# Kernel tuning notes

Measured on AMD Instinct MI355X. Metric: run time of the kernel, lower is better.

Reference implementation:

```python
import jax, jax.numpy as jnp
import numpy as np

B, C, H, W = 4, 512, 64, 64
MID = C // 8  # 64


def setup_inputs() -> dict:
    key = jax.random.key(0)
    ks = jax.random.split(key, 8)
    s = 0.02
    return {
        "x": jax.random.normal(ks[0], (B, C, H, W), dtype=jnp.float32),
        "Wq": jax.random.normal(ks[1], (MID, C), dtype=jnp.float32) * s,
        "bq": jax.random.normal(ks[2], (MID,), dtype=jnp.float32) * s,
        "Wk": jax.random.normal(ks[3], (MID, C), dtype=jnp.float32) * s,
        "bk": jax.random.normal(ks[4], (MID,), dtype=jnp.float32) * s,
        "Wv": jax.random.normal(ks[5], (C, C), dtype=jnp.float32) * s,
        "bv": jax.random.normal(ks[6], (C,), dtype=jnp.float32) * s,
        "gamma": jax.random.uniform(ks[7], (1,), dtype=jnp.float32),
    }


def reference(x, Wq, bq, Wk, bk, Wv, bv, gamma):
    b, c, h, w = x.shape
    n = h * w
    xf = x.reshape(b, c, n)  # [B, C, N]
    # 1x1 convs are per-position linear maps
    q = jnp.einsum('mc,bcn->bnm', Wq, xf) + bq            # [B, N, mid]
    k = jnp.einsum('mc,bcn->bmn', Wk, xf) + bk[:, None]   # [B, mid, N]
    sim = jax.nn.softmax(jnp.einsum('bnm,bmj->bnj', q, k), axis=-1)  # [B, N, N]
    v = jnp.einsum('dc,bcn->bdn', Wv, xf) + bv[:, None]   # [B, C, N]
    # feat[:, d, i] = sum_j v[:, d, j] * sim[:, i, j]
    feat = jnp.einsum('bdj,bij->bdi', v, sim)             # [B, C, N]
    out = gamma[0] * feat + xf
    return out.reshape(b, c, h, w)
```

## Files before the change

### kernel.cpp

```cpp
#include <hip/hip_runtime.h>

#define BATCH 4
#define CCH   512
#define NN    4096
#define MIDD  64

typedef unsigned short u16;
typedef unsigned int   u32;
typedef short s8v  __attribute__((ext_vector_type(8)));
typedef float f16v __attribute__((ext_vector_type(16)));
typedef unsigned int u4v __attribute__((ext_vector_type(4)));

#define L2E 1.44269504088896340736f

__device__ __forceinline__ u16 f2bf(float f) {
  u32 u = __float_as_uint(f);
  u += 0x7fffu + ((u >> 16) & 1u);
  return (u16)(u >> 16);
}

__device__ __forceinline__ void g2lds16(const u16* g, u16* l) {
  __builtin_amdgcn_global_load_lds(
      (const __attribute__((address_space(1))) u32*)(const void*)g,
      (__attribute__((address_space(3))) u32*)(void*)l, 16, 0, 0);
}

#define S_WAITCNT(vm, lgkm) \
  __builtin_amdgcn_s_waitcnt(((vm) & 15) | (((vm) >> 4) << 14) | (0x7 << 4) | ((lgkm) << 8))

__global__ __launch_bounds__(256) void prep_w(
    const float* __restrict__ Wq, const float* __restrict__ Wk,
    const float* __restrict__ Wv, u16* __restrict__ Wb)
{
  int e = (blockIdx.x * 256 + threadIdx.x) * 8;
  const float* src;
  float sc = 1.0f;
  if (e < 64 * 512)       { src = Wq + e; sc = L2E; }
  else if (e < 128 * 512) src = Wk + (e - 64 * 512);
  else                    src = Wv + (e - 128 * 512);
  float4 v0 = *(const float4*)src;
  float4 v1 = *(const float4*)(src + 4);
  uint4 p;
  p.x = (u32)f2bf(sc * v0.x) | ((u32)f2bf(sc * v0.y) << 16);
  p.y = (u32)f2bf(sc * v0.z) | ((u32)f2bf(sc * v0.w) << 16);
  p.z = (u32)f2bf(sc * v1.x) | ((u32)f2bf(sc * v1.y) << 16);
  p.w = (u32)f2bf(sc * v1.z) | ((u32)f2bf(sc * v1.w) << 16);
  *(uint4*)(Wb + e) = p;
}

__global__ __launch_bounds__(256) void transpose_cast(
    const float* __restrict__ x, u16* __restrict__ xbT)
{
  const int b  = blockIdx.z;
  const int c0 = blockIdx.y * 64;
  const int n0 = blockIdx.x * 64;
  const int t  = threadIdx.x;
  __shared__ float ts[64 * 65];

  #pragma unroll
  for (int k = 0; k < 4; k++) {
    int idx = t + 256 * k;
    int cc = idx >> 4, n4 = idx & 15;
    float4 v = *(const float4*)&x[((size_t)(b * CCH + c0 + cc)) * NN + n0 + n4 * 4];
    float* p = &ts[cc * 65 + n4 * 4];
    p[0] = v.x; p[1] = v.y; p[2] = v.z; p[3] = v.w;
  }
  __syncthreads();

  const int n = t >> 2, cb = (t & 3) * 16;
  u16 tmp[16];
  #pragma unroll
  for (int j = 0; j < 16; j++) tmp[j] = f2bf(ts[(cb + j) * 65 + n]);
  u16* dst = &xbT[((size_t)b * NN + n0 + n) * CCH + c0 + cb];
  *(uint4*)&dst[0] = *(uint4*)&tmp[0];
  *(uint4*)&dst[8] = *(uint4*)&tmp[8];
}

__global__ __launch_bounds__(256, 2) void proj_gemm(
    const u16* __restrict__ xbT, const u16* __restrict__ Wb,
    const float* __restrict__ bq, const float* __restrict__ bk,
    const float* __restrict__ bv,
    u16* __restrict__ qT, u16* __restrict__ kT, u16* __restrict__ vF)
{
  const int b  = blockIdx.z;
  const int mt = blockIdx.y;
  const int n0 = blockIdx.x * 256;
  const int t  = threadIdx.x;
  const int ln = t & 31, hi = (t & 63) >> 5, w = t >> 6;
  const int l  = t & 63;
  const int l2 = l & 3, lr = l >> 2;
  const int swc = (l2 ^ (lr & 3)) * 8;

  const int mrow0 = (mt < 8) ? (128 + mt * 64) : ((mt == 8) ? 0 : 64);
  const float* bias = (mt < 8) ? (bv + mt * 64) : ((mt == 8) ? bq : bk);
  const float bsc = (mt == 8) ? L2E : 1.0f;

  __shared__ u16 ws[2][64 * 32];
  __shared__ u16 xs[2][256 * 32];

  const u16* xsrc = xbT + ((size_t)b * NN + n0 + w * 64 + lr) * CCH + swc;
  const u16* wsrc = Wb + (size_t)(mrow0 + w * 16 + lr) * 512 + swc;

  f16v acc[4];
  #pragma unroll
  for (int i = 0; i < 4; i++)
    #pragma unroll
    for (int r = 0; r < 16; r++) acc[i][r] = 0.f;

  #pragma unroll
  for (int i = 0; i < 4; i++)
    g2lds16(xsrc + (size_t)(16 * i) * CCH, &xs[0][(w * 64 + i * 16) * 32]);
  g2lds16(wsrc, &ws[0][w * 16 * 32]);

  for (int it = 0; it < 16; it++) {
    const int cur = it & 1, nxt = cur ^ 1;
    __builtin_amdgcn_s_barrier();
    const int c1 = ((it + 1) & 15) * 32;
    #pragma unroll
    for (int i = 0; i < 4; i++)
      g2lds16(xsrc + (size_t)(16 * i) * CCH + c1, &xs[nxt][(w * 64 + i * 16) * 32]);
    g2lds16(wsrc + c1, &ws[nxt][w * 16 * 32]);

    S_WAITCNT(5, 15);
    __builtin_amdgcn_s_barrier();

    #pragma unroll
    for (int ks = 0; ks < 2; ks++) {
      const int cb = ((2 * ks + hi) ^ (ln & 3)) << 3;
      s8v a0 = *(const s8v*)&ws[cur][(ln)           * 32 + cb];
      s8v a1 = *(const s8v*)&ws[cur][(32 + ln)      * 32 + cb];
      s8v b0 = *(const s8v*)&xs[cur][(w * 64 + ln)      * 32 + cb];
      s8v b1 = *(const s8v*)&xs[cur][(w * 64 + 32 + ln) * 32 + cb];
      acc[0] = __builtin_amdgcn_mfma_f32_32x32x16_bf16(a0, b0, acc[0], 0, 0, 0);
      acc[1] = __builtin_amdgcn_mfma_f32_32x32x16_bf16(a0, b1, acc[1], 0, 0, 0);
      acc[2] = __builtin_amdgcn_mfma_f32_32x32x16_bf16(a1, b0, acc[2], 0, 0, 0);
      acc[3] = __builtin_amdgcn_mfma_f32_32x32x16_bf16(a1, b1, acc[3], 0, 0, 0);
    }
  }

  S_WAITCNT(0, 0);
  __builtin_amdgcn_s_barrier();

  if (mt < 8) {
    u16* xt = &xs[0][0];
    #pragma unroll
    for (int mi = 0; mi < 2; mi++)
      #pragma unroll
      for (int ni = 0; ni < 2; ni++) {
        f16v& a = acc[mi * 2 + ni];
        #pragma unroll
        for (int r = 0; r < 16; r++) {
          int row = (r & 3) + 8 * (r >> 2) + 4 * hi;
          int m   = mi * 32 + row;
          int nr  = w * 64 + ni * 32 + ln;
          int c8  = nr >> 3;
          xt[m * 256 + ((c8 ^ (m & 31)) << 3) + (nr & 7)] = f2bf(a[r] + bias[m]);
        }
      }
    __syncthreads();
    const int jt0 = n0 >> 6;
    const size_t dgb = ((size_t)b * 64 + jt0 + w) * 16 + mt * 2;
    #pragma unroll
    for (int mh = 0; mh < 2; mh++)
      #pragma unroll
      for (int ks = 0; ks < 4; ks++) {
        int c8 = w * 8 + ks * 2 + hi;
        int m  = mh * 32 + ln;
        s8v vv = *(const s8v*)&xt[m * 256 + ((c8 ^ ln) << 3)];
        *(s8v*)&vF[(((dgb + mh) * 4 + ks) * 64 + l) * 8] = vv;
      }
  } else {
    u16* dst = (mt == 8) ? qT : kT;
    u16* xt  = &xs[0][0];
    #pragma unroll
    for (int mi = 0; mi < 2; mi++)
      #pragma unroll
      for (int ni = 0; ni < 2; ni++) {
        f16v& a = acc[mi * 2 + ni];
        #pragma unroll
        for (int r = 0; r < 16; r++) {
          int row = (r & 3) + 8 * (r >> 2) + 4 * hi;
          int m   = mi * 32 + row;
          int nr  = w * 64 + ni * 32 + ln;
          xt[(nr << 6) + (((m >> 3) ^ (ln & 7)) << 3) + (m & 7)] = f2bf(a[r] + bsc * bias[m]);
        }
      }
    __syncthreads();
    const int r7 = t & 7;
    u16* drow = &dst[((size_t)b * NN + n0 + t) * 64];
    #pragma unroll
    for (int k = 0; k < 8; k++)
      *(uint4*)&drow[k * 8] = *(uint4*)&xt[(t << 6) + ((k ^ r7) << 3)];
  }
}

__global__ __launch_bounds__(256, 2) void attn_kernel(
    const u16* __restrict__ qT,
    const u16* __restrict__ kT,
    const u16* __restrict__ vF,
    const float* __restrict__ x,
    const float* __restrict__ gamma,
    float* __restrict__ out)
{
  __shared__ u16 ksm[3][64 * 64];
  __shared__ u4v pex[2][512];

  const int bx    = blockIdx.x;
  const int slot  = bx & 7;
  const int b     = slot >> 1;
  const int dbase = (slot & 1) * 256;
  const int i0    = (bx >> 3) * 64;
  const int t     = threadIdx.x;
  const int l     = t & 63, ln = l & 31, hi = l >> 5;
  const int w     = t >> 6;
  const int qh    = w & 1;
  const int dh    = w >> 1;
  const int l3    = l & 7, lh3 = l >> 3;
  const int sw8   = (l3 ^ lh3) * 8;

  s8v qfrag[4];
  {
    const u16* qp = qT + ((size_t)b * NN + i0 + qh * 32 + ln) * 64 + hi * 8;
    #pragma unroll
    for (int k = 0; k < 4; k++) qfrag[k] = *(const s8v*)(qp + 16 * k);
  }

  const u16* ksrc = kT + (size_t)b * NN * 64 + (size_t)(16 * w + lh3) * 64 + sw8;
  const u16* vfb = vF + (size_t)b * (64 * 16 * 4 * 64 * 8);
  const int dgbase = (slot & 1) * 8 + dh * 4;

  f16v oacc[4];
  #pragma unroll
  for (int i = 0; i < 4; i++)
    #pragma unroll
    for (int r = 0; r < 16; r++) oacc[i][r] = 0.f;
  float lsum = 0.f;

  #pragma unroll
  for (int i = 0; i < 2; i++)
    g2lds16(ksrc + (size_t)(8 * i) * 64, &ksm[0][(w * 2 + i) * 512]);
  #pragma unroll
  for (int i = 0; i < 2; i++)
    g2lds16(ksrc + (size_t)(64 + 8 * i) * 64, &ksm[1][(w * 2 + i) * 512]);

  int cur = 0, nx1 = 1, nx2 = 2;
  for (int it = 0; it < 64; it++) {
    s8v vf[4][4];
    {
      const u16* vp = vfb + (size_t)(it * 16 + dgbase) * 2048 + l * 8;
      #pragma unroll
      for (int dgi = 0; dgi < 4; dgi++)
        #pragma unroll
        for (int ks = 0; ks < 4; ks++)
          vf[dgi][ks] = *(const s8v*)(vp + dgi * 2048 + ks * 512);
    }

    S_WAITCNT(16, 15);
    __builtin_amdgcn_s_barrier();

    {
      const int j2 = ((it + 2) & 63) * 64;
      u16* kdst = &ksm[0][0] + nx2 * 4096 + (w * 2) * 512;
      #pragma unroll
      for (int i = 0; i < 2; i++)
        g2lds16(ksrc + (size_t)(j2 + 8 * i) * 64, kdst + i * 512);
    }

    const u16* kcur = &ksm[0][0] + cur * 4096;
    f16v ssw;
    #pragma unroll
    for (int r = 0; r < 16; r++) ssw[r] = 0.f;
    #pragma unroll
    for (int ks = 0; ks < 4; ks++) {
      s8v kf = *(const s8v*)&kcur[(dh * 32 + ln) * 64 + (((2 * ks + hi) ^ l3) << 3)];
      ssw = __builtin_amdgcn_mfma_f32_32x32x16_bf16(kf, qfrag[ks], ssw, 0, 0, 0);
    }

    float pe[16];
    #pragma unroll
    for (int r = 0; r < 16; r++) {
      pe[r] = __builtin_amdgcn_exp2f(ssw[r]);
      lsum += pe[r];
    }
    u4v own[2];
    #pragma unroll
    for (int b2 = 0; b2 < 2; b2++)
      #pragma unroll
      for (int wd = 0; wd < 2; wd++) {
        u32 X, Y;
        asm("v_cvt_pk_bf16_f32 %0, %1, %2"
            : "=v"(X) : "v"(pe[8 * b2 + 2 * wd]), "v"(pe[8 * b2 + 2 * wd + 1]));
        asm("v_cvt_pk_bf16_f32 %0, %1, %2"
            : "=v"(Y) : "v"(pe[8 * b2 + 4 + 2 * wd]), "v"(pe[8 * b2 + 4 + 2 * wd + 1]));
        u32 T = hi ? X : Y;
        u32 R = (u32)__shfl_xor((int)T, 32);
        own[b2][wd]     = hi ? R : X;
        own[b2][wd + 2] = hi ? Y : R;
      }

    const int pc = it & 1;
    pex[pc][(w * 2 + 0) * 64 + l] = own[0];
    pex[pc][(w * 2 + 1) * 64 + l] = own[1];
    S_WAITCNT(63, 0);
    __builtin_amdgcn_s_barrier();
    u4v o0 = pex[pc][((w ^ 2) * 2 + 0) * 64 + l];
    u4v o1 = pex[pc][((w ^ 2) * 2 + 1) * 64 + l];

    s8v pb0 = (s8v)(dh ? o0 : own[0]);
    s8v pb1 = (s8v)(dh ? o1 : own[1]);
    s8v pb2 = (s8v)(dh ? own[0] : o0);
    s8v pb3 = (s8v)(dh ? own[1] : o1);

    #pragma unroll
    for (int dgi = 0; dgi < 4; dgi++) {
      oacc[dgi] = __builtin_amdgcn_mfma_f32_32x32x16_bf16(vf[dgi][0], pb0, oacc[dgi], 0, 0, 0);
      oacc[dgi] = __builtin_amdgcn_mfma_f32_32x32x16_bf16(vf[dgi][1], pb1, oacc[dgi], 0, 0, 0);
      oacc[dgi] = __builtin_amdgcn_mfma_f32_32x32x16_bf16(vf[dgi][2], pb2, oacc[dgi], 0, 0, 0);
      oacc[dgi] = __builtin_amdgcn_mfma_f32_32x32x16_bf16(vf[dgi][3], pb3, oacc[dgi], 0, 0, 0);
    }

    int tmp = cur; cur = nx1; nx1 = nx2; nx2 = tmp;
  }

  S_WAITCNT(0, 0);
  __builtin_amdgcn_s_barrier();

  float lw = lsum + __shfl_xor(lsum, 32);
  float* lred = (float*)&pex[0][0];
  if (hi == 0) lred[w * 32 + ln] = lw;
  S_WAITCNT(63, 0);
  __builtin_amdgcn_s_barrier();
  const float lt   = lred[w * 32 + ln] + lred[(w ^ 2) * 32 + ln];
  const float linv = 1.0f / lt;
  const float g0   = gamma[0];
  const int   q    = i0 + qh * 32 + ln;
  #pragma unroll
  for (int dgi = 0; dgi < 4; dgi++) {
    f16v& a = oacc[dgi];
    #pragma unroll
    for (int r = 0; r < 16; r++) {
      int dl = dh * 128 + dgi * 32 + (r & 3) + 8 * (r >> 2) + 4 * hi;
      size_t idx = ((size_t)b * CCH + dbase + dl) * NN + q;
      out[idx] = g0 * a[r] * linv + x[idx];
    }
  }
}

extern "C" void kernel_launch(void* const* d_in, const int* in_sizes, int n_in,
                              void* d_out, int out_size, void* d_ws, size_t ws_size,
                              hipStream_t stream) {
  const float* x     = (const float*)d_in[0];
  const float* Wq    = (const float*)d_in[1];
  const float* bq    = (const float*)d_in[2];
  const float* Wk    = (const float*)d_in[3];
  const float* bk    = (const float*)d_in[4];
  const float* Wv    = (const float*)d_in[5];
  const float* bv    = (const float*)d_in[6];
  const float* gamma = (const float*)d_in[7];
  float* out = (float*)d_out;

  u16* qT  = (u16*)d_ws;
  u16* kT  = qT  + (size_t)BATCH * NN * MIDD;
  u16* vF  = kT  + (size_t)BATCH * NN * MIDD;
  u16* xbT = vF  + (size_t)BATCH * CCH * NN;
  u16* Wb  = xbT + (size_t)BATCH * NN * CCH;

  prep_w<<<dim3(160), 256, 0, stream>>>(Wq, Wk, Wv, Wb);
  transpose_cast<<<dim3(NN / 64, CCH / 64, BATCH), 256, 0, stream>>>(x, xbT);
  proj_gemm<<<dim3(NN / 256, 10, BATCH), 256, 0, stream>>>(
      xbT, Wb, bq, bk, bv, qT, kT, vF);
  attn_kernel<<<dim3(512), 256, 0, stream>>>(qT, kT, vF, x, gamma, out);
}
```

Baseline: 231.2 us.

## Double query tile per block and stage V through double-buffered LDS

The attention kernel now uses 512-thread blocks that cover 128 query rows, halving the grid so each K and V tile is shared across twice as many queries. V fragments are staged into a double-buffered LDS buffer with async global-to-LDS loads instead of direct per-wave global loads. The PV MMAs are split so a wave's own P half is consumed before the exchange barrier and the partner's half after it. This cuts redundant V and K global traffic and overlaps MMA work with the exchange, at the cost of more LDS (about 88KB), fewer blocks, and possibly lower occupancy.

```diff
diff --git a/kernel.cpp b/kernel.cpp
--- a/kernel.cpp
+++ b/kernel.cpp
@@ -194,7 +194,7 @@
   }
 }
 
-__global__ __launch_bounds__(256, 2) void attn_kernel(
+__global__ __launch_bounds__(512, 2) void attn_kernel(
     const u16* __restrict__ qT,
     const u16* __restrict__ kT,
     const u16* __restrict__ vF,
@@ -203,18 +203,19 @@
     float* __restrict__ out)
 {
   __shared__ u16 ksm[3][64 * 64];
-  __shared__ u4v pex[2][512];
+  __shared__ u16 vsm[2][32 * 512];
+  __shared__ u4v pex[2][16 * 64];
 
   const int bx    = blockIdx.x;
   const int slot  = bx & 7;
   const int b     = slot >> 1;
   const int dbase = (slot & 1) * 256;
-  const int i0    = (bx >> 3) * 64;
+  const int i0    = (bx >> 3) * 128;
   const int t     = threadIdx.x;
   const int l     = t & 63, ln = l & 31, hi = l >> 5;
   const int w     = t >> 6;
-  const int qh    = w & 1;
-  const int dh    = w >> 1;
+  const int qh    = w & 3;
+  const int dh    = w >> 2;
   const int l3    = l & 7, lh3 = l >> 3;
   const int sw8   = (l3 ^ lh3) * 8;
 
@@ -225,9 +226,9 @@
     for (int k = 0; k < 4; k++) qfrag[k] = *(const s8v*)(qp + 16 * k);
   }
 
-  const u16* ksrc = kT + (size_t)b * NN * 64 + (size_t)(16 * w + lh3) * 64 + sw8;
-  const u16* vfb = vF + (size_t)b * (64 * 16 * 4 * 64 * 8);
-  const int dgbase = (slot & 1) * 8 + dh * 4;
+  const u16* ksrc = kT + (size_t)b * NN * 64 + (size_t)(8 * w + lh3) * 64 + sw8;
+  const u16* vfb = vF + (size_t)b * (64 * 16 * 4 * 64 * 8)
+                      + (size_t)((slot & 1) * 8 + w) * 2048 + l * 8;
 
   f16v oacc[4];
   #pragma unroll
@@ -236,34 +237,24 @@
     for (int r = 0; r < 16; r++) oacc[i][r] = 0.f;
   float lsum = 0.f;
 
-  #pragma unroll
-  for (int i = 0; i < 2; i++)
-    g2lds16(ksrc + (size_t)(8 * i) * 64, &ksm[0][(w * 2 + i) * 512]);
-  #pragma unroll
-  for (int i = 0; i < 2; i++)
-    g2lds16(ksrc + (size_t)(64 + 8 * i) * 64, &ksm[1][(w * 2 + i) * 512]);
-
-  int cur = 0, nx1 = 1, nx2 = 2;
+  g2lds16(ksrc, &ksm[0][w * 512]);
+  #pragma unroll
+  for (int ks = 0; ks < 4; ks++)
+    g2lds16(vfb + ks * 512, &vsm[0][(w * 4 + ks) * 512]);
+  g2lds16(ksrc + (size_t)64 * 64, &ksm[1][w * 512]);
+
+  int cur = 0, nx1 = 1, nx2 = 2, vcur = 0;
   for (int it = 0; it < 64; it++) {
-    s8v vf[4][4];
+    S_WAITCNT(1, 15);
+    __builtin_amdgcn_s_barrier();
+
     {
-      const u16* vp = vfb + (size_t)(it * 16 + dgbase) * 2048 + l * 8;
-      #pragma unroll
-      for (int dgi = 0; dgi < 4; dgi++)
-        #pragma unroll
-        for (int ks = 0; ks < 4; ks++)
-          vf[dgi][ks] = *(const s8v*)(vp + dgi * 2048 + ks * 512);
-    }
-
-    S_WAITCNT(16, 15);
-    __builtin_amdgcn_s_barrier();
-
-    {
+      const u16* vsrc = vfb + (size_t)((it + 1) & 63) * 32768;
+      #pragma unroll
+      for (int ks = 0; ks < 4; ks++)
+        g2lds16(vsrc + ks * 512, &vsm[vcur ^ 1][(w * 4 + ks) * 512]);
       const int j2 = ((it + 2) & 63) * 64;
-      u16* kdst = &ksm[0][0] + nx2 * 4096 + (w * 2) * 512;
-      #pragma unroll
-      for (int i = 0; i < 2; i++)
-        g2lds16(ksrc + (size_t)(j2 + 8 * i) * 64, kdst + i * 512);
+      g2lds16(ksrc + (size_t)j2 * 64, &ksm[0][0] + nx2 * 4096 + w * 512);
     }
 
     const u16* kcur = &ksm[0][0] + cur * 4096;
@@ -301,25 +292,35 @@
     const int pc = it & 1;
     pex[pc][(w * 2 + 0) * 64 + l] = own[0];
     pex[pc][(w * 2 + 1) * 64 + l] = own[1];
+
+    s8v vf[4][4];
+    #pragma unroll
+    for (int dgi = 0; dgi < 4; dgi++)
+      #pragma unroll
+      for (int ks = 0; ks < 4; ks++)
+        vf[dgi][ks] = *(const s8v*)&vsm[vcur][(((dh * 4 + dgi) * 4 + ks) << 9) + l * 8];
+
+    s8v ow0 = (s8v)own[0], ow1 = (s8v)own[1];
+    const int ksa = dh * 2;
+    #pragma unroll
+    for (int dgi = 0; dgi < 4; dgi++) {
+      oacc[dgi] = __builtin_amdgcn_mfma_f32_32x32x16_bf16(vf[dgi][ksa],     ow0, oacc[dgi], 0, 0, 0);
+      oacc[dgi] = __builtin_amdgcn_mfma_f32_32x32x16_bf16(vf[dgi][ksa + 1], ow1, oacc[dgi], 0, 0, 0);
+    }
+
     S_WAITCNT(63, 0);
     __builtin_amdgcn_s_barrier();
-    u4v o0 = pex[pc][((w ^ 2) * 2 + 0) * 64 + l];
-    u4v o1 = pex[pc][((w ^ 2) * 2 + 1) * 64 + l];
-
-    s8v pb0 = (s8v)(dh ? o0 : own[0]);
-    s8v pb1 = (s8v)(dh ? o1 : own[1]);
-    s8v pb2 = (s8v)(dh ? own[0] : o0);
-    s8v pb3 = (s8v)(dh ? own[1] : o1);
-
+    s8v po0 = (s8v)pex[pc][((w ^ 4) * 2 + 0) * 64 + l];
+    s8v po1 = (s8v)pex[pc][((w ^ 4) * 2 + 1) * 64 + l];
+    const int ksb = 2 - ksa;
     #pragma unroll
     for (int dgi = 0; dgi < 4; dgi++) {
-      oacc[dgi] = __builtin_amdgcn_mfma_f32_32x32x16_bf16(vf[dgi][0], pb0, oacc[dgi], 0, 0, 0);
-      oacc[dgi] = __builtin_amdgcn_mfma_f32_32x32x16_bf16(vf[dgi][1], pb1, oacc[dgi], 0, 0, 0);
-      oacc[dgi] = __builtin_amdgcn_mfma_f32_32x32x16_bf16(vf[dgi][2], pb2, oacc[dgi], 0, 0, 0);
-      oacc[dgi] = __builtin_amdgcn_mfma_f32_32x32x16_bf16(vf[dgi][3], pb3, oacc[dgi], 0, 0, 0);
+      oacc[dgi] = __builtin_amdgcn_mfma_f32_32x32x16_bf16(vf[dgi][ksb],     po0, oacc[dgi], 0, 0, 0);
+      oacc[dgi] = __builtin_amdgcn_mfma_f32_32x32x16_bf16(vf[dgi][ksb + 1], po1, oacc[dgi], 0, 0, 0);
     }
 
     int tmp = cur; cur = nx1; nx1 = nx2; nx2 = tmp;
+    vcur ^= 1;
   }
 
   S_WAITCNT(0, 0);
@@ -330,7 +331,7 @@
   if (hi == 0) lred[w * 32 + ln] = lw;
   S_WAITCNT(63, 0);
   __builtin_amdgcn_s_barrier();
-  const float lt   = lred[w * 32 + ln] + lred[(w ^ 2) * 32 + ln];
+  const float lt   = lred[w * 32 + ln] + lred[(w ^ 4) * 32 + ln];
   const float linv = 1.0f / lt;
   const float g0   = gamma[0];
   const int   q    = i0 + qh * 32 + ln;
@@ -369,5 +370,5 @@
   transpose_cast<<<dim3(NN / 64, CCH / 64, BATCH), 256, 0, stream>>>(x, xbT);
   proj_gemm<<<dim3(NN / 256, 10, BATCH), 256, 0, stream>>>(
       xbT, Wb, bq, bk, bv, qT, kT, vF);
-  attn_kernel<<<dim3(512), 256, 0, stream>>>(qT, kT, vF, x, gamma, out);
-}
+  attn_kernel<<<dim3(256), 512, 0, stream>>>(qT, kT, vF, x, gamma, out);
+}
```

After: 639.3 us. +176.5%, slower.
